# Kernel tuning notes

Hardware: AMD Instinct MI355X
Metric: run time of the kernel (lower is better)

The kernel has to match this reference:

```python
import jax, jax.numpy as jnp
import numpy as np
from jax import lax

E = 256


def _channel_attention(x, avg_w, avg_b, max_w, max_b):
    # x: [b,1,N]; 1x1 conv on a [b,1,1,1] tensor is a scalar affine map
    avg = jnp.mean(x, axis=-1, keepdims=True)          # [b,1,1]
    mx = jnp.max(x, axis=-1, keepdims=True)            # [b,1,1]
    a = jax.nn.relu(avg_w[0, 0, 0, 0] * avg + avg_b[0])
    m = jax.nn.relu(max_w[0, 0, 0, 0] * mx + max_b[0])
    return a + m                                        # [b,1,1]


def _spatial_attention(x, sp_w, sp_b):
    # x: [b,1,1]; torch .repeat(1,2,1,1) on a 3D tensor -> [1, 2b, 1, 1]
    x4 = jnp.tile(x[None], (1, 2, 1, 1))                # [1,2b,1,1]
    avg = jnp.mean(x4, axis=1, keepdims=True)           # [1,1,1,1]
    mx = jnp.max(x4, axis=1, keepdims=True)             # [1,1,1,1]
    cat = jnp.concatenate([avg, mx], axis=1)            # [1,2,1,1]
    out = lax.conv_general_dilated(cat, sp_w, (1, 1), [(3, 3), (3, 3)])
    return jax.nn.relu(out + sp_b.reshape(1, 1, 1, 1))  # [1,1,1,1]


def _mha(q_in, k_in, v_in, in_w, in_b, out_w, out_b):
    # torch nn.MultiheadAttention, seq-first layout [L, N, E], num_heads=1
    wq, wk, wv = in_w[:E], in_w[E:2 * E], in_w[2 * E:]
    bq, bk, bv = in_b[:E], in_b[E:2 * E], in_b[2 * E:]
    q = q_in @ wq.T + bq
    k = k_in @ wk.T + bk
    v = v_in @ wv.T + bv                                 # [L,N,E]
    scores = jnp.einsum('lne,mne->nlm', q, k) / jnp.sqrt(jnp.float32(E))
    attn = jax.nn.softmax(scores, axis=-1)               # [N,L,L]
    o = jnp.einsum('nlm,mne->lne', attn, v)              # [L,N,E]
    return o @ out_w.T + out_b


def _gru_cell(x, h, w_ih, w_hh, b_ih, b_hh):
    gi = x @ w_ih.T + b_ih
    gh = h @ w_hh.T + b_hh
    ir, iz, in_ = gi[..., :E], gi[..., E:2 * E], gi[..., 2 * E:]
    hr, hz, hn = gh[..., :E], gh[..., E:2 * E], gh[..., 2 * E:]
    r = jax.nn.sigmoid(ir + hr)
    z = jax.nn.sigmoid(iz + hz)
    n = jnp.tanh(in_ + r * hn)
    return (1.0 - z) * n + z * h


def _ssf(x, ssf_w, ssf_b):
    # x: [b,s,e] -> unsqueeze channel, 7x7 conv, relu -> [b,1,s,e]
    out = lax.conv_general_dilated(x[:, None], ssf_w, (1, 1), [(3, 3), (3, 3)])
    return jax.nn.relu(out + ssf_b.reshape(1, 1, 1, 1))


def setup_inputs() -> dict:
    key = jax.random.key(0)
    ks = jax.random.split(key, 20)
    B, S = 32, 2048
    p = lambda k, shape: jax.random.normal(k, shape, jnp.float32) * 0.05
    return {
        'text_feature': jax.random.normal(ks[0], (B, S, E), jnp.float32),
        'graph_feature': jax.random.normal(ks[1], (B, S, E), jnp.float32),
        'avg_w': p(ks[2], (1, 1, 1, 1)), 'avg_b': p(ks[3], (1,)),
        'max_w': p(ks[4], (1, 1, 1, 1)), 'max_b': p(ks[5], (1,)),
        'sp_w': p(ks[6], (1, 2, 7, 7)), 'sp_b': p(ks[7], (1,)),
        'in_proj_w': p(ks[8], (3 * E, E)), 'in_proj_b': p(ks[9], (3 * E,)),
        'out_w': p(ks[10], (E, E)), 'out_b': p(ks[11], (E,)),
        'lin_w': p(ks[12], (E, E)), 'lin_b': p(ks[13], (E,)),
        'w_ih': p(ks[14], (3 * E, E)), 'w_hh': p(ks[15], (3 * E, E)),
        'b_ih': p(ks[16], (3 * E,)), 'b_hh': p(ks[17], (3 * E,)),
        'ssf_w': p(ks[18], (1, 1, 7, 7)), 'ssf_b': p(ks[19], (1,)),
    }


def reference(text_feature, graph_feature, avg_w, avg_b, max_w, max_b,
              sp_w, sp_b, in_proj_w, in_proj_b, out_w, out_b,
              lin_w, lin_b, w_ih, w_hh, b_ih, b_hh, ssf_w, ssf_b):
    b, s, e = text_feature.shape
    tf4 = text_feature[:, None]                           # [b,1,s,e]
    gf4 = graph_feature[:, None]
    tf_flat = tf4.reshape(b, 1, -1)                       # [b,1,s*e]
    gf_flat = gf4.reshape(b, 1, -1)

    tf_c = _channel_attention(tf_flat, avg_w, avg_b, max_w, max_b)  # [b,1,1]
    gf_c = _channel_attention(gf_flat, avg_w, avg_b, max_w, max_b)

    cross = tf_c @ jnp.swapaxes(gf_c, 1, 2)               # [b,1,1]
    tf_cw = jax.nn.softmax(cross, axis=-1) @ tf_c         # [b,1,1]
    gf_cw = jax.nn.softmax(jnp.swapaxes(cross, 1, 2), axis=-1) @ gf_c

    tf_s = _spatial_attention(tf_cw, sp_w, sp_b)          # [1,1,1,1]
    gf_s = _spatial_attention(gf_cw, sp_w, sp_b)
    norm_tf = jax.nn.softmax(tf_s, axis=2)                # ones (size-1 axis)
    norm_gf = jax.nn.softmax(gf_s, axis=2)

    tf_fused = (tf4 + norm_tf * tf4).reshape(b, s, e)
    gf_fused = (gf4 + norm_gf * gf4).reshape(b, s, e)

    # ESA (fixed call semantics): shared MHA, cross keys
    tf_att = _mha(tf_fused, gf_fused, tf_fused, in_proj_w, in_proj_b, out_w, out_b)
    gf_att = _mha(gf_fused, tf_fused, gf_fused, in_proj_w, in_proj_b, out_w, out_b)

    inter = (tf_att * gf_att) @ lin_w.T + lin_b           # [b,s,e]
    g_tf = _gru_cell(inter, tf_att, w_ih, w_hh, b_ih, b_hh)
    g_gf = _gru_cell(inter, gf_att, w_ih, w_hh, b_ih, b_hh)

    return _ssf(g_tf, ssf_w, ssf_b) + _ssf(g_gf, ssf_w, ssf_b)  # [b,1,s,e]
```

## Files before the change

### kernel.cpp

```cpp
#include <hip/hip_runtime.h>

typedef unsigned short u16;
typedef short s16x8 __attribute__((ext_vector_type(8)));
typedef float f32x4 __attribute__((ext_vector_type(4)));

#define DEVI static __device__ __forceinline__
#define MFMA16(A, B, C) __builtin_amdgcn_mfma_f32_16x16x32_bf16(A, B, C, 0, 0, 0)
#define Z4 ((f32x4){0.f, 0.f, 0.f, 0.f})

DEVI float bf2f(u16 u) {
  __bf16 h; __builtin_memcpy(&h, &u, 2); return (float)h;
}
DEVI u16 f2bf(float f) {
  __bf16 h = (__bf16)f;
  u16 u; __builtin_memcpy(&u, &h, 2); return u;
}
DEVI float rcpf_(float x) { return __builtin_amdgcn_rcpf(x); }
DEVI float sigmoidf_(float x) { return rcpf_(1.0f + __expf(-x)); }
DEVI float tanhf_(float x) { return 1.0f - 2.0f * rcpf_(__expf(2.0f * x) + 1.0f); }

__global__ void k_wconv(const float* __restrict__ w0, const float* __restrict__ w1,
                        const float* __restrict__ w4, u16* __restrict__ out) {
  int c = blockIdx.x * 256 + threadIdx.x;
  if (c >= 57344) return;
  const float* src; long base; int cl;
  if (c < 24576)      { src = w0; base = 0;      cl = c; }
  else if (c < 32768) { src = w1; base = 196608; cl = c - 24576; }
  else                { src = w4; base = 458752; cl = c - 32768; }
  int lr = cl & 15, kg = (cl >> 4) & 3, ks = (cl >> 6) & 7, ct = cl >> 9;
  const float* sp = src + (ct * 16 + lr) * 256 + ks * 32 + kg * 8;
  f32x4 v0 = *(const f32x4*)sp;
  f32x4 v1 = *(const f32x4*)(sp + 4);
  s16x8 t;
  t[0] = (short)f2bf(v0[0]); t[1] = (short)f2bf(v0[1]);
  t[2] = (short)f2bf(v0[2]); t[3] = (short)f2bf(v0[3]);
  t[4] = (short)f2bf(v1[0]); t[5] = (short)f2bf(v1[1]);
  t[6] = (short)f2bf(v1[2]); t[7] = (short)f2bf(v1[3]);
  *(s16x8*)(out + base + (long)cl * 8) = t;
}

__global__ __launch_bounds__(256) void k_wcomb(
    const float* __restrict__ w_ih, const float* __restrict__ lin_w,
    const float* __restrict__ b_lin, const float* __restrict__ b_ih,
    u16* __restrict__ outw, float* __restrict__ outb) {
  __shared__ float row[256];
  int i = blockIdx.x;
  int tid = threadIdx.x;
  row[tid] = w_ih[i * 256 + tid];
  __syncthreads();
  float acc = 0.f;
#pragma unroll 8
  for (int o = 0; o < 256; ++o) acc += row[o] * lin_w[o * 256 + tid];
  int ct = i >> 4, lr = i & 15;
  int ks = tid >> 5, kg = (tid >> 3) & 3, jj = tid & 7;
  long cl = (ct * 8 + ks) * 64 + kg * 16 + lr;
  outw[cl * 8 + jj] = f2bf(acc);
  if (tid == 0) {
    float s = 0.f;
    for (int o = 0; o < 256; ++o) s += row[o] * b_lin[o];
    outb[i] = s + b_ih[i];
  }
}

__global__ void k_tr(const float* __restrict__ text, const float* __restrict__ graph,
                     u16* __restrict__ T2T, u16* __restrict__ T2G) {
  long idx = (long)blockIdx.x * 256 + threadIdx.x;
  int side = (int)(idx >> 21);
  long r = (idx >> 5) & 65535;
  int c8 = (int)(idx & 31);
  long b = r >> 11, s = r & 2047;
  const float* src = (side ? graph : text) + r * 256 + c8 * 8;
  u16* dst = (side ? T2G : T2T) + ((s << 5) + b) * 256 + c8 * 8;
  f32x4 v0 = *(const f32x4*)src;
  f32x4 v1 = *(const f32x4*)(src + 4);
  s16x8 t;
  t[0] = (short)f2bf(2.f * v0[0]); t[1] = (short)f2bf(2.f * v0[1]);
  t[2] = (short)f2bf(2.f * v0[2]); t[3] = (short)f2bf(2.f * v0[3]);
  t[4] = (short)f2bf(2.f * v1[0]); t[5] = (short)f2bf(2.f * v1[1]);
  t[6] = (short)f2bf(2.f * v1[2]); t[7] = (short)f2bf(2.f * v1[3]);
  *(s16x8*)dst = t;
}

#define AOo 0
#define AXo 8448
#define KBo 16896
#define QBo 25344
#define SFo 33792
#define PBo 35904
#define VTo 8448
#define OBo 25344
#define STo 16896

__global__ __launch_bounds__(256, 2) void k_attn(
    const u16* __restrict__ T2T, const u16* __restrict__ T2G,
    const u16* __restrict__ Wproj, const float* __restrict__ bproj,
    const u16* __restrict__ Wout, const float* __restrict__ bout,
    u16* __restrict__ attT, u16* __restrict__ attG) {
  __shared__ u16 sh[37184];
  int n = blockIdx.x, s = blockIdx.y;
  const u16* pown = (s ? T2G : T2T) + n * 8192;
  const u16* poth = (s ? T2T : T2G) + n * 8192;
  u16* dst = s ? attG : attT;
  int tid = threadIdx.x, w = tid >> 6, lane = tid & 63;
  int lr = lane & 15, kg = lane >> 4;
  int fro = ((kg << 4) + lr) * 8;

  {
    int r = tid >> 3, c0 = (tid & 7) * 32;
    const u16* so = pown + r * 256 + c0;
    const u16* sx = poth + r * 256 + c0;
    u16* d0 = sh + AOo + r * 264 + c0;
    u16* d1 = sh + AXo + r * 264 + c0;
#pragma unroll
    for (int j = 0; j < 4; ++j) {
      *(s16x8*)(d0 + j * 8) = *(const s16x8*)(so + j * 8);
      *(s16x8*)(d1 + j * 8) = *(const s16x8*)(sx + j * 8);
    }
  }
  __syncthreads();

  s16x8 af[2][8];

#pragma unroll
  for (int mt = 0; mt < 2; ++mt)
#pragma unroll
    for (int k = 0; k < 8; ++k)
      af[mt][k] = *(const s16x8*)(sh + AXo + (mt * 16 + lr) * 264 + k * 32 + kg * 8);
  for (int i = 0; i < 4; ++i) {
    int ct = 16 + w * 4 + i;
    const u16* wp = Wproj + (ct << 12) + fro;
    s16x8 b[8];
#pragma unroll
    for (int k = 0; k < 8; ++k) b[k] = *(const s16x8*)(wp + (k << 9));
    f32x4 a0 = Z4, a1 = Z4;
#pragma unroll
    for (int k = 0; k < 8; ++k) {
      a0 = MFMA16(af[0][k], b[k], a0);
      a1 = MFMA16(af[1][k], b[k], a1);
    }
    int colk = (ct << 4) + lr;
    float bias = bproj[colk];
    u16* base = sh + KBo + (colk - 256);
#pragma unroll
    for (int j = 0; j < 4; ++j) {
      base[(kg * 4 + j) * 264] = f2bf(a0[j] + bias);
      base[(16 + kg * 4 + j) * 264] = f2bf(a1[j] + bias);
    }
  }

#pragma unroll
  for (int mt = 0; mt < 2; ++mt)
#pragma unroll
    for (int k = 0; k < 8; ++k)
      af[mt][k] = *(const s16x8*)(sh + AOo + (mt * 16 + lr) * 264 + k * 32 + kg * 8);
  for (int i = 0; i < 4; ++i) {
    int ct = w * 4 + i;
    const u16* wp = Wproj + (ct << 12) + fro;
    s16x8 b[8];
#pragma unroll
    for (int k = 0; k < 8; ++k) b[k] = *(const s16x8*)(wp + (k << 9));
    f32x4 a0 = Z4, a1 = Z4;
#pragma unroll
    for (int k = 0; k < 8; ++k) {
      a0 = MFMA16(af[0][k], b[k], a0);
      a1 = MFMA16(af[1][k], b[k], a1);
    }
    int colq = (ct << 4) + lr;
    float bias = bproj[colq];
    u16* base = sh + QBo + colq;
#pragma unroll
    for (int j = 0; j < 4; ++j) {
      base[(kg * 4 + j) * 264] = f2bf(a0[j] + bias);
      base[(16 + kg * 4 + j) * 264] = f2bf(a1[j] + bias);
    }
  }
  __syncthreads();

  {
    int mt = w >> 1, nt = w & 1;
    f32x4 acc = Z4;
#pragma unroll
    for (int k = 0; k < 8; ++k) {
      s16x8 qa = *(const s16x8*)(sh + QBo + (mt * 16 + lr) * 264 + k * 32 + kg * 8);
      s16x8 kb = *(const s16x8*)(sh + KBo + (nt * 16 + lr) * 264 + k * 32 + kg * 8);
      acc = MFMA16(qa, kb, acc);
    }
    float* Sf = (float*)(sh + SFo);
#pragma unroll
    for (int j = 0; j < 4; ++j)
      Sf[(mt * 16 + kg * 4 + j) * 33 + nt * 16 + lr] = acc[j] * 0.0625f;
  }
  __syncthreads();

  for (int i = 0; i < 4; ++i) {
    int ct = 32 + w * 4 + i;
    const u16* wp = Wproj + (ct << 12) + fro;
    s16x8 b[8];
#pragma unroll
    for (int k = 0; k < 8; ++k) b[k] = *(const s16x8*)(wp + (k << 9));
    f32x4 a0 = Z4, a1 = Z4;
#pragma unroll
    for (int k = 0; k < 8; ++k) {
      a0 = MFMA16(af[0][k], b[k], a0);
      a1 = MFMA16(af[1][k], b[k], a1);
    }
    int colv = (ct << 4) + lr;
    float bias = bproj[colv];
    u16* base = sh + VTo + (colv - 512) * 40;
#pragma unroll
    for (int j = 0; j < 4; ++j) {
      base[kg * 4 + j] = f2bf(a0[j] + bias);
      base[16 + kg * 4 + j] = f2bf(a1[j] + bias);
    }
  }
  if (tid < 32) {
    float* Sp = (float*)(sh + SFo) + tid * 33;
    float mx = -1e30f;
#pragma unroll
    for (int m = 0; m < 32; ++m) mx = fmaxf(mx, Sp[m]);
    float e[32]; float sum = 0.f;
#pragma unroll
    for (int m = 0; m < 32; ++m) { e[m] = __expf(Sp[m] - mx); sum += e[m]; }
    float inv = rcpf_(sum);
    u16* Pp = sh + PBo + tid * 40;
#pragma unroll
    for (int m = 0; m < 32; ++m) Pp[m] = f2bf(e[m] * inv);
  }
  __syncthreads();

  {
    s16x8 pa0 = *(const s16x8*)(sh + PBo + lr * 40 + kg * 8);
    s16x8 pa1 = *(const s16x8*)(sh + PBo + (16 + lr) * 40 + kg * 8);
#pragma unroll
    for (int i = 0; i < 4; ++i) {
      int e0 = (w * 4 + i) * 16;
      s16x8 vb = *(const s16x8*)(sh + VTo + (e0 + lr) * 40 + kg * 8);
      f32x4 a0 = MFMA16(pa0, vb, Z4);
      f32x4 a1 = MFMA16(pa1, vb, Z4);
      u16* base = sh + OBo + e0 + lr;
#pragma unroll
      for (int j = 0; j < 4; ++j) {
        base[(kg * 4 + j) * 264] = f2bf(a0[j]);
        base[(16 + kg * 4 + j) * 264] = f2bf(a1[j]);
      }
    }
  }
  __syncthreads();

  {
    s16x8 ao[2][8];
#pragma unroll
    for (int mt = 0; mt < 2; ++mt)
#pragma unroll
      for (int k = 0; k < 8; ++k)
        ao[mt][k] = *(const s16x8*)(sh + OBo + (mt * 16 + lr) * 264 + k * 32 + kg * 8);
    for (int i = 0; i < 4; ++i) {
      int ct = w * 4 + i;
      const u16* wp = Wout + (ct << 12) + fro;
      s16x8 b[8];
#pragma unroll
      for (int k = 0; k < 8; ++k) b[k] = *(const s16x8*)(wp + (k << 9));
      f32x4 a0 = Z4, a1 = Z4;
#pragma unroll
      for (int k = 0; k < 8; ++k) {
        a0 = MFMA16(ao[0][k], b[k], a0);
        a1 = MFMA16(ao[1][k], b[k], a1);
      }
      int cb = (ct << 4) + lr;
      float bias = bout[cb];
      u16* base = sh + STo + cb;
#pragma unroll
      for (int j = 0; j < 4; ++j) {
        base[(kg * 4 + j) * 264] = f2bf(a0[j] + bias);
        base[(16 + kg * 4 + j) * 264] = f2bf(a1[j] + bias);
      }
    }
  }
  __syncthreads();
  {
    int r = tid >> 3, c0 = (tid & 7) * 32;
    u16* dr = dst + ((long)n << 13) + r * 256 + c0;
#pragma unroll
    for (int j = 0; j < 4; ++j)
      *(s16x8*)(dr + j * 8) = *(const s16x8*)(sh + STo + r * 264 + c0 + j * 8);
  }
}

__global__ __launch_bounds__(512, 1) void k_gru(
    const u16* __restrict__ attT, const u16* __restrict__ attG,
    const u16* __restrict__ Wcomb, const float* __restrict__ bcomb,
    const u16* __restrict__ Whh, const float* __restrict__ bhh,
    u16* __restrict__ g1, u16* __restrict__ g2) {
  __shared__ u16 sh[25344];
  const int AT = 0, AG = 8448, HI = 16896;
  int m0 = blockIdx.x * 32;
  int tid = threadIdx.x, w = tid >> 6, lane = tid & 63;
  int lr = lane & 15, kg = lane >> 4;
  int fro = ((kg << 4) + lr) * 8;

  {
    int r = tid >> 4, c0 = (tid & 15) * 16;
    const u16* pt = attT + (m0 + r) * 256 + c0;
    const u16* pg = attG + (m0 + r) * 256 + c0;
    *(s16x8*)(sh + AT + r * 264 + c0) = __builtin_nontemporal_load((const s16x8*)pt);
    *(s16x8*)(sh + AT + r * 264 + c0 + 8) = __builtin_nontemporal_load((const s16x8*)(pt + 8));
    *(s16x8*)(sh + AG + r * 264 + c0) = __builtin_nontemporal_load((const s16x8*)pg);
    *(s16x8*)(sh + AG + r * 264 + c0 + 8) = __builtin_nontemporal_load((const s16x8*)(pg + 8));
  }
  __syncthreads();

  {
    int r = tid >> 4, c0 = (tid & 15) * 16;
#pragma unroll
    for (int half = 0; half < 2; ++half) {
      s16x8 t8 = *(const s16x8*)(sh + AT + r * 264 + c0 + half * 8);
      s16x8 g8 = *(const s16x8*)(sh + AG + r * 264 + c0 + half * 8);
      s16x8 h;
#pragma unroll
      for (int j = 0; j < 8; ++j)
        h[j] = (short)f2bf(bf2f((u16)t8[j]) * bf2f((u16)g8[j]));
      *(s16x8*)(sh + HI + r * 264 + c0 + half * 8) = h;
    }
  }
  __syncthreads();

#define LDGATE(slot, kk) { \
    int fo_ = ((kk) << 9) + fro; \
    bI[slot][0] = *(const s16x8*)(Wcomb + (ct0 << 12) + fo_); \
    bI[slot][1] = *(const s16x8*)(Wcomb + (ct1 << 12) + fo_); \
    bI[slot][2] = *(const s16x8*)(Wcomb + (ct2 << 12) + fo_); \
    bH[slot][0] = *(const s16x8*)(Whh + (ct0 << 12) + fo_); \
    bH[slot][1] = *(const s16x8*)(Whh + (ct1 << 12) + fo_); \
    bH[slot][2] = *(const s16x8*)(Whh + (ct2 << 12) + fo_); }

  s16x8 o1b[2], o2b[2];
#pragma unroll
  for (int ic = 0; ic < 2; ++ic) {
    int ct0 = w * 2 + ic, ct1 = 16 + ct0, ct2 = 32 + ct0;
    int col = (ct0 << 4) + lr;
    f32x4 acc[3][3][2];
#pragma unroll
    for (int g = 0; g < 3; ++g)
#pragma unroll
      for (int s2 = 0; s2 < 3; ++s2) { acc[g][s2][0] = Z4; acc[g][s2][1] = Z4; }
    s16x8 bI[2][3], bH[2][3];
    LDGATE(0, 0)
#pragma unroll
    for (int k = 0; k < 8; ++k) {
      const int c = k & 1, nx = c ^ 1;
      if (k < 7) { LDGATE(nx, k + 1) }
      int ko = k * 32 + kg * 8;
      s16x8 aI0 = *(const s16x8*)(sh + HI + lr * 264 + ko);
      s16x8 aI1 = *(const s16x8*)(sh + HI + (16 + lr) * 264 + ko);
      s16x8 aT0 = *(const s16x8*)(sh + AT + lr * 264 + ko);
      s16x8 aT1 = *(const s16x8*)(sh + AT + (16 + lr) * 264 + ko);
      s16x8 aG0 = *(const s16x8*)(sh + AG + lr * 264 + ko);
      s16x8 aG1 = *(const s16x8*)(sh + AG + (16 + lr) * 264 + ko);
#pragma unroll
      for (int g = 0; g < 3; ++g) {
        acc[g][0][0] = MFMA16(aI0, bI[c][g], acc[g][0][0]);
        acc[g][0][1] = MFMA16(aI1, bI[c][g], acc[g][0][1]);
        acc[g][1][0] = MFMA16(aT0, bH[c][g], acc[g][1][0]);
        acc[g][1][1] = MFMA16(aT1, bH[c][g], acc[g][1][1]);
        acc[g][2][0] = MFMA16(aG0, bH[c][g], acc[g][2][0]);
        acc[g][2][1] = MFMA16(aG1, bH[c][g], acc[g][2][1]);
      }
    }
    float bir = bcomb[col], biz = bcomb[col + 256], bin_ = bcomb[col + 512];
    float bhr = bhh[col], bhz = bhh[col + 256], bhn = bhh[col + 512];
    s16x8 o1v, o2v;
#pragma unroll
    for (int mt = 0; mt < 2; ++mt)
#pragma unroll
      for (int j = 0; j < 4; ++j) {
        int row = mt * 16 + kg * 4 + j;
        float hT = bf2f(sh[AT + row * 264 + col]);
        float hG = bf2f(sh[AG + row * 264 + col]);
        float ir = acc[0][0][mt][j] + bir;
        float iz = acc[1][0][mt][j] + biz;
        float inn = acc[2][0][mt][j] + bin_;
        float r1 = sigmoidf_(ir + acc[0][1][mt][j] + bhr);
        float z1 = sigmoidf_(iz + acc[1][1][mt][j] + bhz);
        float n1 = tanhf_(inn + r1 * (acc[2][1][mt][j] + bhn));
        o1v[mt * 4 + j] = (short)f2bf((1.f - z1) * n1 + z1 * hT);
        float r2 = sigmoidf_(ir + acc[0][2][mt][j] + bhr);
        float z2 = sigmoidf_(iz + acc[1][2][mt][j] + bhz);
        float n2 = tanhf_(inn + r2 * (acc[2][2][mt][j] + bhn));
        o2v[mt * 4 + j] = (short)f2bf((1.f - z2) * n2 + z2 * hG);
      }
    o1b[ic] = o1v; o2b[ic] = o2v;
  }
  __syncthreads();

#pragma unroll
  for (int ic = 0; ic < 2; ++ic) {
    int col = ((w * 2 + ic) << 4) + lr;
#pragma unroll
    for (int mt = 0; mt < 2; ++mt)
#pragma unroll
      for (int j = 0; j < 4; ++j) {
        int row = mt * 16 + kg * 4 + j;
        sh[AT + row * 264 + col] = (u16)o1b[ic][mt * 4 + j];
        sh[AG + row * 264 + col] = (u16)o2b[ic][mt * 4 + j];
      }
  }
  __syncthreads();
  {
    int r = tid >> 4, c0 = (tid & 15) * 16;
    u16* p1 = g1 + (long)(m0 + r) * 256 + c0;
    u16* p2 = g2 + (long)(m0 + r) * 256 + c0;
    *(s16x8*)(p1) = *(const s16x8*)(sh + AT + r * 264 + c0);
    *(s16x8*)(p1 + 8) = *(const s16x8*)(sh + AT + r * 264 + c0 + 8);
    *(s16x8*)(p2) = *(const s16x8*)(sh + AG + r * 264 + c0);
    *(s16x8*)(p2 + 8) = *(const s16x8*)(sh + AG + r * 264 + c0 + 8);
  }
}

__global__ __launch_bounds__(256) void k_conv(
    const u16* __restrict__ g1, const u16* __restrict__ g2,
    const float* __restrict__ wss, const float* __restrict__ bss,
    float* __restrict__ out) {
  __shared__ float s1[38][73];
  __shared__ float s2[38][73];
  int et = blockIdx.x, st = blockIdx.y, b = blockIdx.z;
  int s0 = st * 32, e0 = et * 64;
  int tid = threadIdx.x;
  for (int idx = tid; idx < 38 * 70; idx += 256) {
    int r = idx / 70, c = idx % 70;
    int s = s0 + r - 3, e = e0 + c - 3;
    float v1 = 0.f, v2 = 0.f;
    if (s >= 0 && s < 2048 && e >= 0 && e < 256) {
      long off = ((long)s * 32 + b) * 256 + e;
      v1 = bf2f(g1[off]); v2 = bf2f(g2[off]);
    }
    s1[r][c] = v1; s2[r][c] = v2;
  }
  __syncthreads();
  float bias = bss[0];
  int oy = tid >> 3, ox = (tid & 7) * 8;
  float a1[8] = {0.f, 0.f, 0.f, 0.f, 0.f, 0.f, 0.f, 0.f};
  float a2[8] = {0.f, 0.f, 0.f, 0.f, 0.f, 0.f, 0.f, 0.f};
#pragma unroll
  for (int ky = 0; ky < 7; ++ky) {
    float wr[7];
#pragma unroll
    for (int kx = 0; kx < 7; ++kx) wr[kx] = wss[ky * 7 + kx];
    float r1[14], r2[14];
#pragma unroll
    for (int j = 0; j < 14; ++j) { r1[j] = s1[oy + ky][ox + j]; r2[j] = s2[oy + ky][ox + j]; }
#pragma unroll
    for (int x = 0; x < 8; ++x)
#pragma unroll
      for (int kx = 0; kx < 7; ++kx) {
        a1[x] += r1[x + kx] * wr[kx];
        a2[x] += r2[x + kx] * wr[kx];
      }
  }
  long obase = ((long)b * 2048 + s0 + oy) * 256 + e0 + ox;
  f32x4 o0, o1;
#pragma unroll
  for (int x = 0; x < 4; ++x) {
    o0[x] = fmaxf(a1[x] + bias, 0.f) + fmaxf(a2[x] + bias, 0.f);
    o1[x] = fmaxf(a1[x + 4] + bias, 0.f) + fmaxf(a2[x + 4] + bias, 0.f);
  }
  *(f32x4*)(out + obase) = o0;
  *(f32x4*)(out + obase + 4) = o1;
}

extern "C" void kernel_launch(void* const* d_in, const int* in_sizes, int n_in,
                              void* d_out, int out_size, void* d_ws, size_t ws_size,
                              hipStream_t stream) {
  const float* text = (const float*)d_in[0];
  const float* graph = (const float*)d_in[1];
  const float* in_proj_w = (const float*)d_in[8];
  const float* in_proj_b = (const float*)d_in[9];
  const float* out_w = (const float*)d_in[10];
  const float* out_b = (const float*)d_in[11];
  const float* lin_w = (const float*)d_in[12];
  const float* lin_b = (const float*)d_in[13];
  const float* w_ih = (const float*)d_in[14];
  const float* w_hh = (const float*)d_in[15];
  const float* b_ih = (const float*)d_in[16];
  const float* b_hh = (const float*)d_in[17];
  const float* ssf_w = (const float*)d_in[18];
  const float* ssf_b = (const float*)d_in[19];

  u16* g1 = (u16*)d_ws;
  u16* g2 = g1 + 16777216;
  u16* T2T = g1;
  u16* T2G = g2;
  u16* Wall = g2 + 16777216;
  u16* Wproj = Wall;
  u16* Wout = Wall + 196608;
  u16* Wcomb = Wall + 262144;
  u16* Whh = Wall + 458752;
  float* bcomb = (float*)(Wall + 655360);

  u16* attT = (u16*)d_out;
  u16* attG = attT + 16777216;

  k_wconv<<<224, 256, 0, stream>>>(in_proj_w, out_w, w_hh, Wall);
  k_wcomb<<<768, 256, 0, stream>>>(w_ih, lin_w, lin_b, b_ih, Wcomb, bcomb);
  k_tr<<<16384, 256, 0, stream>>>(text, graph, T2T, T2G);

  k_attn<<<dim3(2048, 2), 256, 0, stream>>>(T2T, T2G, Wproj, in_proj_b, Wout, out_b, attT, attG);
  k_gru<<<2048, 512, 0, stream>>>(attT, attG, Wcomb, bcomb, Whh, b_hh, g1, g2);
  k_conv<<<dim3(4, 64, 32), 256, 0, stream>>>(g1, g2, ssf_w, ssf_b, (float*)d_out);
}
```

Before: 375.9 us.

## Fuse input transpose, attention and GRU into one kernel per sequence position

Merges the transpose/convert kernel, the attention kernel and the GRU kernel into a single 512-thread kernel. Each block loads both text and graph rows for one sequence position straight from fp32 global memory, runs both attention directions in parallel wave groups, and feeds the attention outputs from shared memory directly into the GRU stage. This removes the global round trips for the transposed bf16 inputs and the attention outputs. The cost is a much larger shared-memory footprint (about 145KB) and one block per CU, which lowers occupancy and the ability to hide latency.

Measured after the change: 447.5 us. +19.1%, slower.

```diff
diff --git a/kernel.cpp b/kernel.cpp
--- a/kernel.cpp
+++ b/kernel.cpp
@@ -62,62 +62,54 @@
   }
 }
 
-__global__ void k_tr(const float* __restrict__ text, const float* __restrict__ graph,
-                     u16* __restrict__ T2T, u16* __restrict__ T2G) {
-  long idx = (long)blockIdx.x * 256 + threadIdx.x;
-  int side = (int)(idx >> 21);
-  long r = (idx >> 5) & 65535;
-  int c8 = (int)(idx & 31);
-  long b = r >> 11, s = r & 2047;
-  const float* src = (side ? graph : text) + r * 256 + c8 * 8;
-  u16* dst = (side ? T2G : T2T) + ((s << 5) + b) * 256 + c8 * 8;
-  f32x4 v0 = *(const f32x4*)src;
-  f32x4 v1 = *(const f32x4*)(src + 4);
-  s16x8 t;
-  t[0] = (short)f2bf(2.f * v0[0]); t[1] = (short)f2bf(2.f * v0[1]);
-  t[2] = (short)f2bf(2.f * v0[2]); t[3] = (short)f2bf(2.f * v0[3]);
-  t[4] = (short)f2bf(2.f * v1[0]); t[5] = (short)f2bf(2.f * v1[1]);
-  t[6] = (short)f2bf(2.f * v1[2]); t[7] = (short)f2bf(2.f * v1[3]);
-  *(s16x8*)dst = t;
-}
-
-#define AOo 0
-#define AXo 8448
-#define KBo 16896
-#define QBo 25344
-#define SFo 33792
-#define PBo 35904
-#define VTo 8448
-#define OBo 25344
-#define STo 16896
-
-__global__ __launch_bounds__(256, 2) void k_attn(
-    const u16* __restrict__ T2T, const u16* __restrict__ T2G,
+#define PTo 0
+#define PGo 8448
+#define ATo 57472
+#define AGo 65920
+#define HIo 16896
+
+__global__ __launch_bounds__(512, 1) void k_fused(
+    const float* __restrict__ text, const float* __restrict__ graph,
     const u16* __restrict__ Wproj, const float* __restrict__ bproj,
     const u16* __restrict__ Wout, const float* __restrict__ bout,
-    u16* __restrict__ attT, u16* __restrict__ attG) {
-  __shared__ u16 sh[37184];
-  int n = blockIdx.x, s = blockIdx.y;
-  const u16* pown = (s ? T2G : T2T) + n * 8192;
-  const u16* poth = (s ? T2T : T2G) + n * 8192;
-  u16* dst = s ? attG : attT;
+    const u16* __restrict__ Wcomb, const float* __restrict__ bcomb,
+    const u16* __restrict__ Whh, const float* __restrict__ bhh,
+    u16* __restrict__ g1, u16* __restrict__ g2) {
+  __shared__ u16 sh[74368];
+  int s = blockIdx.x;
   int tid = threadIdx.x, w = tid >> 6, lane = tid & 63;
   int lr = lane & 15, kg = lane >> 4;
   int fro = ((kg << 4) + lr) * 8;
-
-  {
-    int r = tid >> 3, c0 = (tid & 7) * 32;
-    const u16* so = pown + r * 256 + c0;
-    const u16* sx = poth + r * 256 + c0;
-    u16* d0 = sh + AOo + r * 264 + c0;
-    u16* d1 = sh + AXo + r * 264 + c0;
+  int sw = w >> 2, wq = w & 3;
+
+  {
+    int sd = tid >> 8;
+    int t2 = tid & 255;
+    int r = t2 >> 3, c0 = (t2 & 7) * 32;
+    const float* src = (sd ? graph : text) + ((long)r * 2048 + s) * 256 + c0;
+    u16* dst = sh + (sd ? PGo : PTo) + r * 264 + c0;
 #pragma unroll
     for (int j = 0; j < 4; ++j) {
-      *(s16x8*)(d0 + j * 8) = *(const s16x8*)(so + j * 8);
-      *(s16x8*)(d1 + j * 8) = *(const s16x8*)(sx + j * 8);
-    }
-  }
-  __syncthreads();
+      f32x4 v0 = *(const f32x4*)(src + j * 8);
+      f32x4 v1 = *(const f32x4*)(src + j * 8 + 4);
+      s16x8 t;
+      t[0] = (short)f2bf(2.f * v0[0]); t[1] = (short)f2bf(2.f * v0[1]);
+      t[2] = (short)f2bf(2.f * v0[2]); t[3] = (short)f2bf(2.f * v0[3]);
+      t[4] = (short)f2bf(2.f * v1[0]); t[5] = (short)f2bf(2.f * v1[1]);
+      t[6] = (short)f2bf(2.f * v1[2]); t[7] = (short)f2bf(2.f * v1[3]);
+      *(s16x8*)(dst + j * 8) = t;
+    }
+  }
+  __syncthreads();
+
+  int owno = sw ? PGo : PTo;
+  int otho = sw ? PTo : PGo;
+  int Qs = 16896 + sw * 16896;
+  int Ks = Qs + 8448;
+  int VTs = Qs;
+  int PBs = 54912 + sw * 1280;
+  int OBs = sw * 8448;
+  int ATTs = sw ? AGo : ATo;
 
   s16x8 af[2][8];
 
@@ -125,9 +117,9 @@
   for (int mt = 0; mt < 2; ++mt)
 #pragma unroll
     for (int k = 0; k < 8; ++k)
-      af[mt][k] = *(const s16x8*)(sh + AXo + (mt * 16 + lr) * 264 + k * 32 + kg * 8);
+      af[mt][k] = *(const s16x8*)(sh + otho + (mt * 16 + lr) * 264 + k * 32 + kg * 8);
   for (int i = 0; i < 4; ++i) {
-    int ct = 16 + w * 4 + i;
+    int ct = 16 + wq * 4 + i;
     const u16* wp = Wproj + (ct << 12) + fro;
     s16x8 b[8];
 #pragma unroll
@@ -140,7 +132,7 @@
     }
     int colk = (ct << 4) + lr;
     float bias = bproj[colk];
-    u16* base = sh + KBo + (colk - 256);
+    u16* base = sh + Ks + (colk - 256);
 #pragma unroll
     for (int j = 0; j < 4; ++j) {
       base[(kg * 4 + j) * 264] = f2bf(a0[j] + bias);
@@ -152,9 +144,9 @@
   for (int mt = 0; mt < 2; ++mt)
 #pragma unroll
     for (int k = 0; k < 8; ++k)
-      af[mt][k] = *(const s16x8*)(sh + AOo + (mt * 16 + lr) * 264 + k * 32 + kg * 8);
+      af[mt][k] = *(const s16x8*)(sh + owno + (mt * 16 + lr) * 264 + k * 32 + kg * 8);
   for (int i = 0; i < 4; ++i) {
-    int ct = w * 4 + i;
+    int ct = wq * 4 + i;
     const u16* wp = Wproj + (ct << 12) + fro;
     s16x8 b[8];
 #pragma unroll
@@ -167,7 +159,7 @@
     }
     int colq = (ct << 4) + lr;
     float bias = bproj[colq];
-    u16* base = sh + QBo + colq;
+    u16* base = sh + Qs + colq;
 #pragma unroll
     for (int j = 0; j < 4; ++j) {
       base[(kg * 4 + j) * 264] = f2bf(a0[j] + bias);
@@ -177,15 +169,15 @@
   __syncthreads();
 
   {
-    int mt = w >> 1, nt = w & 1;
+    int mt = wq >> 1, nt = wq & 1;
     f32x4 acc = Z4;
 #pragma unroll
     for (int k = 0; k < 8; ++k) {
-      s16x8 qa = *(const s16x8*)(sh + QBo + (mt * 16 + lr) * 264 + k * 32 + kg * 8);
-      s16x8 kb = *(const s16x8*)(sh + KBo + (nt * 16 + lr) * 264 + k * 32 + kg * 8);
+      s16x8 qa = *(const s16x8*)(sh + Qs + (mt * 16 + lr) * 264 + k * 32 + kg * 8);
+      s16x8 kb = *(const s16x8*)(sh + Ks + (nt * 16 + lr) * 264 + k * 32 + kg * 8);
       acc = MFMA16(qa, kb, acc);
     }
-    float* Sf = (float*)(sh + SFo);
+    float* Sf = (float*)(sh + 50688 + sw * 2112);
 #pragma unroll
     for (int j = 0; j < 4; ++j)
       Sf[(mt * 16 + kg * 4 + j) * 33 + nt * 16 + lr] = acc[j] * 0.0625f;
@@ -193,7 +185,7 @@
   __syncthreads();
 
   for (int i = 0; i < 4; ++i) {
-    int ct = 32 + w * 4 + i;
+    int ct = 32 + wq * 4 + i;
     const u16* wp = Wproj + (ct << 12) + fro;
     s16x8 b[8];
 #pragma unroll
@@ -206,15 +198,16 @@
     }
     int colv = (ct << 4) + lr;
     float bias = bproj[colv];
-    u16* base = sh + VTo + (colv - 512) * 40;
+    u16* base = sh + VTs + (colv - 512) * 40;
 #pragma unroll
     for (int j = 0; j < 4; ++j) {
       base[kg * 4 + j] = f2bf(a0[j] + bias);
       base[16 + kg * 4 + j] = f2bf(a1[j] + bias);
     }
   }
-  if (tid < 32) {
-    float* Sp = (float*)(sh + SFo) + tid * 33;
+  if ((tid & 255) < 32) {
+    int sd = tid >> 8, l = tid & 31;
+    float* Sp = (float*)(sh + 50688 + sd * 2112) + l * 33;
     float mx = -1e30f;
 #pragma unroll
     for (int m = 0; m < 32; ++m) mx = fmaxf(mx, Sp[m]);
@@ -222,22 +215,22 @@
 #pragma unroll
     for (int m = 0; m < 32; ++m) { e[m] = __expf(Sp[m] - mx); sum += e[m]; }
     float inv = rcpf_(sum);
-    u16* Pp = sh + PBo + tid * 40;
+    u16* Pp = sh + 54912 + sd * 1280 + l * 40;
 #pragma unroll
     for (int m = 0; m < 32; ++m) Pp[m] = f2bf(e[m] * inv);
   }
   __syncthreads();
 
   {
-    s16x8 pa0 = *(const s16x8*)(sh + PBo + lr * 40 + kg * 8);
-    s16x8 pa1 = *(const s16x8*)(sh + PBo + (16 + lr) * 40 + kg * 8);
+    s16x8 pa0 = *(const s16x8*)(sh + PBs + lr * 40 + kg * 8);
+    s16x8 pa1 = *(const s16x8*)(sh + PBs + (16 + lr) * 40 + kg * 8);
 #pragma unroll
     for (int i = 0; i < 4; ++i) {
-      int e0 = (w * 4 + i) * 16;
-      s16x8 vb = *(const s16x8*)(sh + VTo + (e0 + lr) * 40 + kg * 8);
+      int e0 = (wq * 4 + i) * 16;
+      s16x8 vb = *(const s16x8*)(sh + VTs + (e0 + lr) * 40 + kg * 8);
       f32x4 a0 = MFMA16(pa0, vb, Z4);
       f32x4 a1 = MFMA16(pa1, vb, Z4);
-      u16* base = sh + OBo + e0 + lr;
+      u16* base = sh + OBs + e0 + lr;
 #pragma unroll
       for (int j = 0; j < 4; ++j) {
         base[(kg * 4 + j) * 264] = f2bf(a0[j]);
@@ -253,9 +246,9 @@
     for (int mt = 0; mt < 2; ++mt)
 #pragma unroll
       for (int k = 0; k < 8; ++k)
-        ao[mt][k] = *(const s16x8*)(sh + OBo + (mt * 16 + lr) * 264 + k * 32 + kg * 8);
+        ao[mt][k] = *(const s16x8*)(sh + OBs + (mt * 16 + lr) * 264 + k * 32 + kg * 8);
     for (int i = 0; i < 4; ++i) {
-      int ct = w * 4 + i;
+      int ct = wq * 4 + i;
       const u16* wp = Wout + (ct << 12) + fro;
       s16x8 b[8];
 #pragma unroll
@@ -268,7 +261,7 @@
       }
       int cb = (ct << 4) + lr;
       float bias = bout[cb];
-      u16* base = sh + STo + cb;
+      u16* base = sh + ATTs + cb;
 #pragma unroll
       for (int j = 0; j < 4; ++j) {
         base[(kg * 4 + j) * 264] = f2bf(a0[j] + bias);
@@ -277,49 +270,18 @@
     }
   }
   __syncthreads();
-  {
-    int r = tid >> 3, c0 = (tid & 7) * 32;
-    u16* dr = dst + ((long)n << 13) + r * 256 + c0;
-#pragma unroll
-    for (int j = 0; j < 4; ++j)
-      *(s16x8*)(dr + j * 8) = *(const s16x8*)(sh + STo + r * 264 + c0 + j * 8);
-  }
-}
-
-__global__ __launch_bounds__(512, 1) void k_gru(
-    const u16* __restrict__ attT, const u16* __restrict__ attG,
-    const u16* __restrict__ Wcomb, const float* __restrict__ bcomb,
-    const u16* __restrict__ Whh, const float* __restrict__ bhh,
-    u16* __restrict__ g1, u16* __restrict__ g2) {
-  __shared__ u16 sh[25344];
-  const int AT = 0, AG = 8448, HI = 16896;
-  int m0 = blockIdx.x * 32;
-  int tid = threadIdx.x, w = tid >> 6, lane = tid & 63;
-  int lr = lane & 15, kg = lane >> 4;
-  int fro = ((kg << 4) + lr) * 8;
 
   {
     int r = tid >> 4, c0 = (tid & 15) * 16;
-    const u16* pt = attT + (m0 + r) * 256 + c0;
-    const u16* pg = attG + (m0 + r) * 256 + c0;
-    *(s16x8*)(sh + AT + r * 264 + c0) = __builtin_nontemporal_load((const s16x8*)pt);
-    *(s16x8*)(sh + AT + r * 264 + c0 + 8) = __builtin_nontemporal_load((const s16x8*)(pt + 8));
-    *(s16x8*)(sh + AG + r * 264 + c0) = __builtin_nontemporal_load((const s16x8*)pg);
-    *(s16x8*)(sh + AG + r * 264 + c0 + 8) = __builtin_nontemporal_load((const s16x8*)(pg + 8));
-  }
-  __syncthreads();
-
-  {
-    int r = tid >> 4, c0 = (tid & 15) * 16;
 #pragma unroll
     for (int half = 0; half < 2; ++half) {
-      s16x8 t8 = *(const s16x8*)(sh + AT + r * 264 + c0 + half * 8);
-      s16x8 g8 = *(const s16x8*)(sh + AG + r * 264 + c0 + half * 8);
+      s16x8 t8 = *(const s16x8*)(sh + ATo + r * 264 + c0 + half * 8);
+      s16x8 g8 = *(const s16x8*)(sh + AGo + r * 264 + c0 + half * 8);
       s16x8 h;
 #pragma unroll
       for (int j = 0; j < 8; ++j)
         h[j] = (short)f2bf(bf2f((u16)t8[j]) * bf2f((u16)g8[j]));
-      *(s16x8*)(sh + HI + r * 264 + c0 + half * 8) = h;
+      *(s16x8*)(sh + HIo + r * 264 + c0 + half * 8) = h;
     }
   }
   __syncthreads();
@@ -350,12 +312,12 @@
       const int c = k & 1, nx = c ^ 1;
       if (k < 7) { LDGATE(nx, k + 1) }
       int ko = k * 32 + kg * 8;
-      s16x8 aI0 = *(const s16x8*)(sh + HI + lr * 264 + ko);
-      s16x8 aI1 = *(const s16x8*)(sh + HI + (16 + lr) * 264 + ko);
-      s16x8 aT0 = *(const s16x8*)(sh + AT + lr * 264 + ko);
-      s16x8 aT1 = *(const s16x8*)(sh + AT + (16 + lr) * 264 + ko);
-      s16x8 aG0 = *(const s16x8*)(sh + AG + lr * 264 + ko);
-      s16x8 aG1 = *(const s16x8*)(sh + AG + (16 + lr) * 264 + ko);
+      s16x8 aI0 = *(const s16x8*)(sh + HIo + lr * 264 + ko);
+      s16x8 aI1 = *(const s16x8*)(sh + HIo + (16 + lr) * 264 + ko);
+      s16x8 aT0 = *(const s16x8*)(sh + ATo + lr * 264 + ko);
+      s16x8 aT1 = *(const s16x8*)(sh + ATo + (16 + lr) * 264 + ko);
+      s16x8 aG0 = *(const s16x8*)(sh + AGo + lr * 264 + ko);
+      s16x8 aG1 = *(const s16x8*)(sh + AGo + (16 + lr) * 264 + ko);
 #pragma unroll
       for (int g = 0; g < 3; ++g) {
         acc[g][0][0] = MFMA16(aI0, bI[c][g], acc[g][0][0]);
@@ -374,8 +336,8 @@
 #pragma unroll
       for (int j = 0; j < 4; ++j) {
         int row = mt * 16 + kg * 4 + j;
-        float hT = bf2f(sh[AT + row * 264 + col]);
-        float hG = bf2f(sh[AG + row * 264 + col]);
+        float hT = bf2f(sh[ATo + row * 264 + col]);
+        float hG = bf2f(sh[AGo + row * 264 + col]);
         float ir = acc[0][0][mt][j] + bir;
         float iz = acc[1][0][mt][j] + biz;
         float inn = acc[2][0][mt][j] + bin_;
@@ -400,19 +362,20 @@
 #pragma unroll
       for (int j = 0; j < 4; ++j) {
         int row = mt * 16 + kg * 4 + j;
-        sh[AT + row * 264 + col] = (u16)o1b[ic][mt * 4 + j];
-        sh[AG + row * 264 + col] = (u16)o2b[ic][mt * 4 + j];
+        sh[ATo + row * 264 + col] = (u16)o1b[ic][mt * 4 + j];
+        sh[AGo + row * 264 + col] = (u16)o2b[ic][mt * 4 + j];
       }
   }
   __syncthreads();
   {
     int r = tid >> 4, c0 = (tid & 15) * 16;
-    u16* p1 = g1 + (long)(m0 + r) * 256 + c0;
-    u16* p2 = g2 + (long)(m0 + r) * 256 + c0;
-    *(s16x8*)(p1) = *(const s16x8*)(sh + AT + r * 264 + c0);
-    *(s16x8*)(p1 + 8) = *(const s16x8*)(sh + AT + r * 264 + c0 + 8);
-    *(s16x8*)(p2) = *(const s16x8*)(sh + AG + r * 264 + c0);
-    *(s16x8*)(p2 + 8) = *(const s16x8*)(sh + AG + r * 264 + c0 + 8);
+    long m0 = (long)s * 32;
+    u16* p1 = g1 + (m0 + r) * 256 + c0;
+    u16* p2 = g2 + (m0 + r) * 256 + c0;
+    *(s16x8*)(p1) = *(const s16x8*)(sh + ATo + r * 264 + c0);
+    *(s16x8*)(p1 + 8) = *(const s16x8*)(sh + ATo + r * 264 + c0 + 8);
+    *(s16x8*)(p2) = *(const s16x8*)(sh + AGo + r * 264 + c0);
+    *(s16x8*)(p2 + 8) = *(const s16x8*)(sh + AGo + r * 264 + c0 + 8);
   }
 }
 
@@ -487,8 +450,6 @@
 
   u16* g1 = (u16*)d_ws;
   u16* g2 = g1 + 16777216;
-  u16* T2T = g1;
-  u16* T2G = g2;
   u16* Wall = g2 + 16777216;
   u16* Wproj = Wall;
   u16* Wout = Wall + 196608;
@@ -496,14 +457,10 @@
   u16* Whh = Wall + 458752;
   float* bcomb = (float*)(Wall + 655360);
 
-  u16* attT = (u16*)d_out;
-  u16* attG = attT + 16777216;
-
   k_wconv<<<224, 256, 0, stream>>>(in_proj_w, out_w, w_hh, Wall);
   k_wcomb<<<768, 256, 0, stream>>>(w_ih, lin_w, lin_b, b_ih, Wcomb, bcomb);
-  k_tr<<<16384, 256, 0, stream>>>(text, graph, T2T, T2G);
-
-  k_attn<<<dim3(2048, 2), 256, 0, stream>>>(T2T, T2G, Wproj, in_proj_b, Wout, out_b, attT, attG);
-  k_gru<<<2048, 512, 0, stream>>>(attT, attG, Wcomb, bcomb, Whh, b_hh, g1, g2);
+
+  k_fused<<<2048, 512, 0, stream>>>(text, graph, Wproj, in_proj_b, Wout, out_b,
+                                    Wcomb, bcomb, Whh, b_hh, g1, g2);
   k_conv<<<dim3(4, 64, 32), 256, 0, stream>>>(g1, g2, ssf_w, ssf_b, (float*)d_out);
 }
```
